# Kernel optimization log

Hardware: AMD Instinct MI355X
Metric: run time of the kernel (lower is better)

The kernel has to match this reference:

```python
import jax, jax.numpy as jnp
import numpy as np

B, N, D = 64, 512, 768


def setup_inputs() -> dict:
    key = jax.random.key(0)
    k = jax.random.split(key, 7)
    x = jax.random.normal(k[0], (B, N, D), dtype=jnp.float32)
    adj = jax.random.normal(k[1], (B, N, N), dtype=jnp.float32)
    # additive BERT-style mask: 0 for valid tokens, -10000 for padding
    lengths = jax.random.randint(k[2], (B,), N // 2, N + 1)
    valid = jnp.arange(N)[None, :] < lengths[:, None]          # [B, N]
    mask = jnp.where(valid, 0.0, -10000.0).astype(jnp.float32).reshape(B, 1, 1, N)
    roots_label = (jax.random.uniform(k[3], (B, N)) < 0.1).astype(jnp.float32)
    root_mask = valid.astype(jnp.int32)
    w_root = jax.random.normal(k[4], (D,), dtype=jnp.float32) / np.sqrt(D)
    b_root = jnp.zeros((), dtype=jnp.float32)
    return {"x": x, "adj": adj, "mask": mask, "roots_label": roots_label,
            "root_mask": root_mask, "w_root": w_root, "b_root": b_root}


def _matrix_tree_multi(scores, root):
    # scores: [B,N,N], root: [B,N]
    A = jnp.exp(scores)
    R = jnp.exp(root)
    L = jnp.sum(A, axis=1)                     # column sums (torch dim=1)
    LL = jnp.zeros_like(A).at[:, jnp.arange(A.shape[1]), jnp.arange(A.shape[1])].set(L + R) - A
    # equivalent to diag(L) - A + diag(R); keep diag of -A zeroed by set:
    LL = (jnp.apply_along_axis(jnp.diag, 1, np.zeros((1,))) if False else LL)  # no-op
    LL = jax.vmap(jnp.diag)(L + R) - A + jax.vmap(jnp.diag)(jnp.diagonal(A, axis1=1, axis2=2))
    # Recompute cleanly to match torch exactly: LL = diag(L) - A + diag(R)
    LL = jax.vmap(jnp.diag)(L) - A + jax.vmap(jnp.diag)(R)
    LL_inv = jnp.linalg.inv(LL)                # [B,N,N]
    LL_inv_diag = jnp.diagonal(LL_inv, axis1=1, axis2=2)   # [B,N]
    d0 = R * LL_inv_diag                       # root marginals [B,N]
    tmp1 = A * LL_inv_diag[:, None, :]         # A[i,j] * diag[j]
    tmp2 = A * jnp.swapaxes(LL_inv, 1, 2)      # A[i,j] * LL_inv[j,i]
    d = tmp1 - tmp2                            # edge marginals [B,N,N]
    return d, d0


def reference(x, adj, mask, roots_label, root_mask, w_root, b_root):
    root = jnp.einsum("bnd,d->bn", x, w_root) + b_root          # [B,N]
    m = mask[:, 0] / -10000.0                                    # [B,1,N], 0 valid / 1 pad
    root = jnp.maximum(root - m[:, 0, :] * 50.0, -40.0)
    scores = adj - m * 50.0 - jnp.swapaxes(m, 1, 2) * 50.0
    scores = jnp.maximum(scores, -40.0)
    d, d0 = _matrix_tree_multi(scores, root)
    # BCE root loss
    active = root_mask.reshape(-1) == 1
    labels = jnp.where(active, roots_label.reshape(-1), 0.0).astype(jnp.float32)
    logits = jnp.clip(d0.reshape(-1), 1e-5, 1.0 - 1e-5).astype(jnp.float32)
    bce = -(labels * jnp.log(logits) + (1.0 - labels) * jnp.log(1.0 - logits))
    loss_root = jnp.mean(bce * root_mask.reshape(-1).astype(jnp.float32))
    # attention = d^T with padded key columns zeroed
    attn = jnp.swapaxes(d, 1, 2)
    pad = jnp.broadcast_to(m.astype(bool), scores.shape)         # [B,N,N]
    attn = jnp.where(pad, 0.0, attn)
    context = jnp.matmul(attn, x)                                # [B,N,D]
    return context, d, loss_root
```

## Files before the change

### kernel.cpp

```cpp
#include <hip/hip_runtime.h>
#include <cstdint>
#include <cstddef>

#define BB 64
#define NN 512
#define DD 768
#define KB 64
#define NSTEP (NN/KB)

typedef __bf16 bf16x8 __attribute__((ext_vector_type(8)));
typedef float f32x4 __attribute__((ext_vector_type(4)));
typedef unsigned short us8 __attribute__((ext_vector_type(8)));
typedef double f64x4 __attribute__((ext_vector_type(4)));
typedef double f64x2 __attribute__((ext_vector_type(2)));

__device__ __forceinline__ float aval(float adjv, float mi, float mj) {
    return expf(fmaxf(adjv - 50.f * (mi + mj), -40.f));
}

__device__ __forceinline__ unsigned short f2bf(float v) {
    union { float f; unsigned int u; } c; c.f = v;
    return (unsigned short)((c.u + 0x7fffu + ((c.u >> 16) & 1u)) >> 16);
}
__device__ __forceinline__ float bf2f(unsigned short h) {
    union { unsigned int u; float f; } c; c.u = ((unsigned int)h) << 16;
    return c.f;
}

__device__ __forceinline__ void gl_lds16(const void* g, void* l) {
    __builtin_amdgcn_global_load_lds((const __attribute__((address_space(1))) unsigned int*)g,
                                     (__attribute__((address_space(3))) unsigned int*)l, 16, 0, 0);
}

__global__ void k_root(const float* __restrict__ x, const float* __restrict__ mask,
                       const float* __restrict__ w, const float* __restrict__ br,
                       float* __restrict__ R) {
    int wave = threadIdx.x >> 6, lane = threadIdx.x & 63;
    int row = blockIdx.x * 4 + wave;
    const float* xr = x + (size_t)row * DD;
    float s = 0.f;
#pragma unroll
    for (int k = 0; k < DD / 64; ++k) s += xr[k * 64 + lane] * w[k * 64 + lane];
    for (int off = 32; off; off >>= 1) s += __shfl_down(s, off, 64);
    if (lane == 0) {
        float m = mask[row] * -1e-4f;
        float rv = fmaxf(s + br[0] - 50.f * m, -40.f);
        R[row] = expf(rv);
    }
}

__global__ void k_colsum(const float* __restrict__ adj, const float* __restrict__ mask,
                         double* __restrict__ Lp) {
    int b = blockIdx.x, chunk = blockIdx.y;
    int j = threadIdx.x;
    float mj = mask[b * NN + j] * -1e-4f;
    const float* ab = adj + (size_t)b * NN * NN;
    double acc = 0.0;
    int i0 = chunk * 128;
    for (int i = i0; i < i0 + 128; ++i) {
        float mi = mask[b * NN + i] * -1e-4f;
        acc += (double)aval(ab[(size_t)i * NN + j], mi, mj);
    }
    Lp[((size_t)b * 4 + chunk) * NN + j] = acc;
}

template <typename T>
__global__ void k_build(const float* __restrict__ adj, const float* __restrict__ mask,
                        const float* __restrict__ R, const double* __restrict__ Lp,
                        T* __restrict__ M) {
    int b = blockIdx.x >> 9;
    int r = blockIdx.x & 511;
    int c = threadIdx.x;
    float mr = mask[b * NN + r] * -1e-4f;
    float mc = mask[b * NN + c] * -1e-4f;
    size_t idx = ((size_t)b * NN + r) * NN + c;
    float a = aval(adj[idx], mr, mc);
    T v;
    if (r == c) {
        const double* lp = Lp + (size_t)b * 4 * NN;
        double L = lp[c] + lp[NN + c] + lp[2 * NN + c] + lp[3 * NN + c];
        v = (T)(L - (double)a + (double)R[b * NN + c]);
    } else {
        v = (T)(-a);
    }
    M[idx] = v;
}

template <typename T>
__global__ void k_savecol(const T* __restrict__ M, T* __restrict__ Cb, int k0) {
    int t = threadIdx.x;
    int c = t & 63, rr = t >> 6;
    int row = blockIdx.x * 4 + rr;
    int b = row >> 9, i = row & 511;
    Cb[(size_t)row * KB + c] = M[((size_t)b * NN + i) * NN + k0 + c];
}

template <typename T>
__global__ void k_invblk(const T* __restrict__ M, T* __restrict__ Bb, int k0) {
    __shared__ double pr[KB];
    __shared__ double fv[KB];
    __shared__ double pvt;
    int b = blockIdx.x;
    int r = threadIdx.x & 63, q = threadIdx.x >> 6;
    double a[16];
    const T* Mb = M + ((size_t)b * NN + k0) * NN + k0;
#pragma unroll
    for (int c = 0; c < 16; ++c) a[c] = (double)Mb[(size_t)r * NN + q * 16 + c];
    for (int k = 0; k < KB; ++k) {
        int kq = k >> 4, kc = k & 15;
        if (r == k && q == kq) pvt = a[kc];
        __syncthreads();
        double ip = 1.0 / pvt;
        if (r == k) {
#pragma unroll
            for (int c = 0; c < 16; ++c) a[c] *= ip;
            if (q == kq) a[kc] = ip;
#pragma unroll
            for (int c = 0; c < 16; ++c) pr[q * 16 + c] = a[c];
        }
        if (r != k && q == kq) fv[r] = a[kc];
        __syncthreads();
        if (r != k) {
            double f = fv[r];
#pragma unroll
            for (int c = 0; c < 16; ++c) a[c] -= f * pr[q * 16 + c];
            if (q == kq) a[kc] = -f * ip;
        }
        __syncthreads();
    }
    T* Bo = Bb + (size_t)b * KB * KB;
#pragma unroll
    for (int c = 0; c < 16; ++c) Bo[r * KB + q * 16 + c] = (T)a[c];
}

__global__ __launch_bounds__(256) void k_piv_mfma(double* __restrict__ M,
                                                  const double* __restrict__ Bb, int step) {
    __shared__ double Ms[64][66];
    int b = blockIdx.y, jt = blockIdx.x;
    int t = threadIdx.x, w = t >> 6, l = t & 63;
    double* Mb = M + (size_t)b * NN * NN;
    double* Pr = Mb + (size_t)(step * 64) * NN;
    const double* Bi = Bb + (size_t)b * KB * KB;
    if (jt == step) {
        for (int i = 0; i < 16; ++i) {
            int c = i * 256 + t;
            int row = c >> 6, col = c & 63;
            Pr[(size_t)row * NN + step * 64 + col] = Bi[row * 64 + col];
        }
        return;
    }
    const double* Mg = Pr + jt * 64;
    for (int i = 0; i < 8; ++i) {
        int c = i * 256 + t;
        int row = c >> 5, ch = c & 31;
        f64x2 v = *(const f64x2*)(Mg + (size_t)row * NN + ch * 2);
        Ms[row][ch * 2] = v[0]; Ms[row][ch * 2 + 1] = v[1];
    }
    __syncthreads();
    int lr = l & 15, lg = l >> 4;
    double a[16];
#pragma unroll
    for (int kk = 0; kk < 16; ++kk) a[kk] = Bi[(w * 16 + lr) * 64 + kk * 4 + lg];
    double* Og = Pr + (size_t)(w * 16) * NN + jt * 64;
#pragma unroll
    for (int cf = 0; cf < 4; ++cf) {
        f64x4 acc = {0., 0., 0., 0.};
#pragma unroll
        for (int kk = 0; kk < 16; ++kk)
            acc = __builtin_amdgcn_mfma_f64_16x16x4f64(a[kk], Ms[kk * 4 + lg][cf * 16 + lr], acc, 0, 0, 0);
#pragma unroll
        for (int r = 0; r < 4; ++r) Og[(size_t)(lg + 4 * r) * NN + cf * 16 + lr] = acc[r];
    }
}

__global__ __launch_bounds__(256) void k_upd2(double* __restrict__ M,
                                              const double* __restrict__ Bb, int step) {
    __shared__ double Ts[64][66];
    int b = blockIdx.y;
    int x = blockIdx.x;
    int it = x >> 1, half = x & 1;
    if (it >= step) ++it;
    int t = threadIdx.x, w = t >> 6, l = t & 63;
    double* Mb = M + (size_t)b * NN * NN;
    {
        const double* Cg = Mb + (size_t)(it * 64) * NN + step * 64;
        for (int i = 0; i < 8; ++i) {
            int c = i * 256 + t;
            int row = c >> 5, ch = c & 31;
            f64x2 v = *(const f64x2*)(Cg + (size_t)row * NN + ch * 2);
            Ts[row][ch * 2] = -v[0]; Ts[row][ch * 2 + 1] = -v[1];
        }
    }
    __syncthreads();
    int lr = l & 15, lg = l >> 4;
    double a[16];
#pragma unroll
    for (int kk = 0; kk < 16; ++kk) a[kk] = Ts[w * 16 + lr][kk * 4 + lg];
    __syncthreads();
    int nj = half ? 3 : 4;
    for (int jj = 0; jj < nj; ++jj) {
        int jtidx = half ? 4 + jj : jj;
        int jt = (jtidx < step) ? jtidx : jtidx + 1;
        const double* Rg = Mb + (size_t)(step * 64) * NN + jt * 64;
        for (int i = 0; i < 8; ++i) {
            int c = i * 256 + t;
            int row = c >> 5, ch = c & 31;
            f64x2 v = *(const f64x2*)(Rg + (size_t)row * NN + ch * 2);
            Ts[row][ch * 2] = v[0]; Ts[row][ch * 2 + 1] = v[1];
        }
        __syncthreads();
        double* Og = Mb + (size_t)(it * 64 + w * 16) * NN + jt * 64;
#pragma unroll
        for (int cf = 0; cf < 4; ++cf) {
            int c0 = cf * 16 + lr;
            f64x4 acc;
#pragma unroll
            for (int r = 0; r < 4; ++r) acc[r] = Og[(size_t)(lg + 4 * r) * NN + c0];
#pragma unroll
            for (int kk = 0; kk < 16; ++kk)
                acc = __builtin_amdgcn_mfma_f64_16x16x4f64(a[kk], Ts[kk * 4 + lg][c0], acc, 0, 0, 0);
#pragma unroll
            for (int r = 0; r < 4; ++r) Og[(size_t)(lg + 4 * r) * NN + c0] = acc[r];
        }
        __syncthreads();
    }
    if (half) {
        const double* Bi = Bb + (size_t)b * KB * KB;
        for (int i = 0; i < 8; ++i) {
            int c = i * 256 + t;
            int row = c >> 5, ch = c & 31;
            f64x2 v = *(const f64x2*)(Bi + row * 64 + ch * 2);
            Ts[row][ch * 2] = v[0]; Ts[row][ch * 2 + 1] = v[1];
        }
        __syncthreads();
        double* Og = Mb + (size_t)(it * 64 + w * 16) * NN + step * 64;
#pragma unroll
        for (int cf = 0; cf < 4; ++cf) {
            int c0 = cf * 16 + lr;
            f64x4 acc = {0., 0., 0., 0.};
#pragma unroll
            for (int kk = 0; kk < 16; ++kk)
                acc = __builtin_amdgcn_mfma_f64_16x16x4f64(a[kk], Ts[kk * 4 + lg][c0], acc, 0, 0, 0);
#pragma unroll
            for (int r = 0; r < 4; ++r) Og[(size_t)(lg + 4 * r) * NN + c0] = acc[r];
        }
    }
}

template <typename T>
__global__ void k_pivrows(T* __restrict__ M, const T* __restrict__ Bb, int k0) {
    __shared__ double Bi[KB][KB];
    __shared__ double Mt[KB][KB + 1];
    int b = blockIdx.x, jt = blockIdx.y * 64;
    const T* Bo = Bb + (size_t)b * KB * KB;
    T* Mb = M + ((size_t)b * NN + k0) * NN;
    int t = threadIdx.x;
    for (int e = t; e < KB * KB; e += 256) {
        int rr = e >> 6, cc = e & 63;
        Bi[rr][cc] = (double)Bo[e];
        Mt[rr][cc] = (double)Mb[(size_t)rr * NN + jt + cc];
    }
    __syncthreads();
    if (blockIdx.y == (unsigned)(k0 >> 6)) {
        for (int e = t; e < KB * KB; e += 256) {
            int rr = e >> 6, cc = e & 63;
            Mb[(size_t)rr * NN + jt + cc] = (T)Bi[rr][cc];
        }
        return;
    }
    int tx = t & 15, ty = t >> 4;
    double acc[4][4] = {};
    for (int k = 0; k < KB; ++k) {
        double av[4], bv[4];
#pragma unroll
        for (int u = 0; u < 4; ++u) { av[u] = Bi[ty * 4 + u][k]; bv[u] = Mt[k][tx * 4 + u]; }
#pragma unroll
        for (int u = 0; u < 4; ++u)
#pragma unroll
            for (int v = 0; v < 4; ++v) acc[u][v] += av[u] * bv[v];
    }
#pragma unroll
    for (int u = 0; u < 4; ++u)
#pragma unroll
        for (int v = 0; v < 4; ++v)
            Mb[(size_t)(ty * 4 + u) * NN + jt + tx * 4 + v] = (T)acc[u][v];
}

template <typename T>
__global__ void k_update(T* __restrict__ M, const T* __restrict__ Cb, int k0) {
    int step = k0 >> 6;
    int it = blockIdx.y;
    if (it == step) return;
    int b = blockIdx.x, jt = blockIdx.z;
    __shared__ double Ct[KB][KB + 1];
    __shared__ double Rt[KB][KB + 1];
    int t = threadIdx.x;
    const T* Cbb = Cb + ((size_t)b * NN + it * 64) * KB;
    const T* Rb  = M + ((size_t)b * NN + k0) * NN + jt * 64;
    for (int e = t; e < KB * KB; e += 256) {
        int rr = e >> 6, cc = e & 63;
        Ct[rr][cc] = (double)Cbb[(size_t)rr * KB + cc];
        Rt[rr][cc] = (double)Rb[(size_t)rr * NN + cc];
    }
    __syncthreads();
    int tx = t & 15, ty = t >> 4;
    double acc[4][4] = {};
    for (int k = 0; k < KB; ++k) {
        double av[4], bv[4];
#pragma unroll
        for (int u = 0; u < 4; ++u) { av[u] = Ct[ty * 4 + u][k]; bv[u] = Rt[k][tx * 4 + u]; }
#pragma unroll
        for (int u = 0; u < 4; ++u)
#pragma unroll
            for (int v = 0; v < 4; ++v) acc[u][v] += av[u] * bv[v];
    }
    T* Mo = M + ((size_t)b * NN + it * 64) * NN + jt * 64;
    bool blockcol = (jt == step);
#pragma unroll
    for (int u = 0; u < 4; ++u) {
        int row = ty * 4 + u;
#pragma unroll
        for (int v = 0; v < 4; ++v) {
            int col = tx * 4 + v;
            double val = (double)Mo[(size_t)row * NN + col] - acc[u][v];
            if (blockcol) val -= Ct[row][col];
            Mo[(size_t)row * NN + col] = (T)val;
        }
    }
}

template <typename T>
__global__ void k_dgloss(const T* __restrict__ M, const float* __restrict__ R,
                         const float* __restrict__ rlab, const int* __restrict__ rmask,
                         double* __restrict__ Dg, float* __restrict__ lossp) {
    int idx = blockIdx.x * 256 + threadIdx.x;
    int b = idx >> 9, n = idx & 511;
    double xv = (double)M[((size_t)b * NN + n) * NN + n];
    Dg[idx] = xv;
    float d0 = R[idx] * (float)xv;
    float lg = fminf(fmaxf(d0, 1e-5f), 1.f - 1e-5f);
    float rm = (float)rmask[idx];
    float lab = (rmask[idx] == 1) ? rlab[idx] : 0.f;
    float bce = -(lab * logf(lg) + (1.f - lab) * logf(1.f - lg));
    __shared__ double sm[256];
    sm[threadIdx.x] = (double)(bce * rm);
    __syncthreads();
    for (int s = 128; s; s >>= 1) {
        if (threadIdx.x < s) sm[threadIdx.x] += sm[threadIdx.x + s];
        __syncthreads();
    }
    if (threadIdx.x == 0) lossp[blockIdx.x] = (float)sm[0];
}

__global__ void k_lossfin(const float* __restrict__ lossp, float* __restrict__ outv) {
    __shared__ double sm[128];
    sm[threadIdx.x] = (double)lossp[threadIdx.x];
    __syncthreads();
    for (int s = 64; s; s >>= 1) {
        if (threadIdx.x < s) sm[threadIdx.x] += sm[threadIdx.x + s];
        __syncthreads();
    }
    if (threadIdx.x == 0) outv[0] = (float)(sm[0] / (double)(BB * NN));
}

template <typename T>
__global__ void k_d(const T* __restrict__ M, const double* __restrict__ Dg,
                    const float* __restrict__ adj, const float* __restrict__ mask,
                    float* __restrict__ dout) {
    int b = blockIdx.x, i0 = blockIdx.y * 64, j0 = blockIdx.z * 64;
    __shared__ double Xt[64][65];
    int t = threadIdx.x, ii = t & 63, jj0 = t >> 6;
    const T* Mb = M + (size_t)b * NN * NN;
    for (int jj = jj0; jj < 64; jj += 4)
        Xt[jj][ii] = (double)Mb[(size_t)(j0 + jj) * NN + i0 + ii];
    __syncthreads();
    int jc = t & 63, ir0 = t >> 6;
    float mj = mask[b * NN + j0 + jc] * -1e-4f;
    double dg = Dg[b * NN + j0 + jc];
    const float* ab = adj + (size_t)b * NN * NN;
    float* db = dout + (size_t)b * NN * NN;
    for (int ir = ir0; ir < 64; ir += 4) {
        int i = i0 + ir;
        float mi = mask[b * NN + i] * -1e-4f;
        float a = aval(ab[(size_t)i * NN + j0 + jc], mi, mj);
        db[(size_t)i * NN + j0 + jc] = a * (float)(dg - Xt[jc][ir]);
    }
}

template <typename T>
__global__ void k_d2(const T* __restrict__ M, const double* __restrict__ Dg,
                     const float* __restrict__ adj, const float* __restrict__ mask,
                     float* __restrict__ dout,
                     unsigned short* __restrict__ ATh, unsigned short* __restrict__ ATl) {
    int b = blockIdx.x, i0 = blockIdx.y * 64, j0 = blockIdx.z * 64;
    __shared__ float Xt[64][65];
    __shared__ float dt[64][65];
    int t = threadIdx.x, ii = t & 63, jj0 = t >> 6;
    const T* Mb = M + (size_t)b * NN * NN;
    for (int jj = jj0; jj < 64; jj += 4)
        Xt[jj][ii] = (float)Mb[(size_t)(j0 + jj) * NN + i0 + ii];
    __syncthreads();
    int jc = t & 63, ir0 = t >> 6;
    float mj = mask[b * NN + j0 + jc] * -1e-4f;
    double dg = Dg[b * NN + j0 + jc];
    const float* ab = adj + (size_t)b * NN * NN;
    float* db = dout + (size_t)b * NN * NN;
    for (int ir = ir0; ir < 64; ir += 4) {
        int i = i0 + ir;
        float mi = mask[b * NN + i] * -1e-4f;
        float a = aval(ab[(size_t)i * NN + j0 + jc], mi, mj);
        float v = a * (float)(dg - (double)Xt[jc][ir]);
        db[(size_t)i * NN + j0 + jc] = v;
        dt[ir][jc] = v;
    }
    __syncthreads();
    int ql = t >> 2, kq = t & 3;
    us8 vh0, vh1, vl0, vl1;
#pragma unroll
    for (int u = 0; u < 16; ++u) {
        int k = kq * 16 + u;
        float mk = mask[b * NN + i0 + k] * -1e-4f;
        float v = (mk > 0.5f) ? 0.f : dt[k][ql];
        unsigned short h = f2bf(v);
        unsigned short lo = f2bf(v - bf2f(h));
        if (u < 8) { vh0[u] = h; vl0[u] = lo; } else { vh1[u - 8] = h; vl1[u - 8] = lo; }
    }
    size_t ao = ((size_t)b * NN + j0 + ql) * NN + i0 + kq * 16;
    *(us8*)&ATh[ao] = vh0; *(us8*)&ATh[ao + 8] = vh1;
    *(us8*)&ATl[ao] = vl0; *(us8*)&ATl[ao + 8] = vl1;
}

__global__ void k_cvt_x(const float* __restrict__ x,
                        unsigned short* __restrict__ XTh, unsigned short* __restrict__ XTl) {
    int b = blockIdx.x, k0 = blockIdx.y * 64, c0 = blockIdx.z * 64;
    __shared__ float xs[64][65];
    int t = threadIdx.x;
#pragma unroll
    for (int rep = 0; rep < 16; ++rep) {
        int e = rep * 256 + t;
        int row = e >> 6, col = e & 63;
        xs[row][col] = x[((size_t)b * NN + k0 + row) * DD + c0 + col];
    }
    __syncthreads();
    int cl = t >> 2, kq = t & 3;
    us8 vh0, vh1, vl0, vl1;
#pragma unroll
    for (int u = 0; u < 16; ++u) {
        int k = kq * 16 + u;
        float v = xs[k][cl];
        unsigned short h = f2bf(v);
        unsigned short lo = f2bf(v - bf2f(h));
        if (u < 8) { vh0[u] = h; vl0[u] = lo; } else { vh1[u - 8] = h; vl1[u - 8] = lo; }
    }
    size_t ao = ((size_t)b * DD + c0 + cl) * NN + k0 + kq * 16;
    *(us8*)&XTh[ao] = vh0; *(us8*)&XTh[ao + 8] = vh1;
    *(us8*)&XTl[ao] = vl0; *(us8*)&XTl[ao + 8] = vl1;
}

__global__ __launch_bounds__(256) void k_ctx3(const unsigned short* __restrict__ ATh,
                                              const unsigned short* __restrict__ ATl,
                                              const unsigned short* __restrict__ XTh,
                                              const unsigned short* __restrict__ XTl,
                                              float* __restrict__ ctx) {
    __shared__ __align__(16) unsigned short ABs[128 * 64];
    __shared__ __align__(16) unsigned short Xs[128 * 64];
    int b = blockIdx.x;
    int bm = blockIdx.y * 128, bn = blockIdx.z * 128;
    int t = threadIdx.x, wid = t >> 6, lane = t & 63;
    f32x4 acc[4][4];
#pragma unroll
    for (int i = 0; i < 4; ++i)
#pragma unroll
        for (int j = 0; j < 4; ++j) acc[i][j] = (f32x4){0.f, 0.f, 0.f, 0.f};

    const unsigned short* Agh = ATh + ((size_t)b * NN + bm) * NN;
    const unsigned short* Agl = ATl + ((size_t)b * NN + bm) * NN;
    const unsigned short* Xgh = XTh + ((size_t)b * DD + bn) * NN;
    const unsigned short* Xgl = XTl + ((size_t)b * DD + bn) * NN;

    int m0 = (wid >> 1) * 64, n0 = (wid & 1) * 64;
    int kc = lane >> 4;

    for (int kt = 0; kt < 16; ++kt) {
        int ki = kt * 32;
        __syncthreads();
#pragma unroll
        for (int it2 = 0; it2 < 4; ++it2) {
            int chunk = it2 * 256 + wid * 64 + lane;
            int row = chunk >> 3;
            int gs = (chunk & 7) ^ (row & 7);
            const unsigned short* s = (gs < 4) ? Agh + (size_t)row * NN + ki + gs * 8
                                               : Agl + (size_t)row * NN + ki + (gs - 4) * 8;
            gl_lds16(s, &ABs[(it2 * 256 + wid * 64) * 8]);
        }
#pragma unroll
        for (int it2 = 0; it2 < 4; ++it2) {
            int chunk = it2 * 256 + wid * 64 + lane;
            int row = chunk >> 3;
            int gs = (chunk & 7) ^ (row & 7);
            const unsigned short* s = (gs < 4) ? Xgh + (size_t)row * NN + ki + gs * 8
                                               : Xgl + (size_t)row * NN + ki + (gs - 4) * 8;
            gl_lds16(s, &Xs[(it2 * 256 + wid * 64) * 8]);
        }
        __syncthreads();
        bf16x8 ah[4], al[4], xh[4], xl[4];
#pragma unroll
        for (int f = 0; f < 4; ++f) {
            int ar = m0 + f * 16 + (lane & 15);
            ah[f] = *(const bf16x8*)&ABs[(ar * 8 + (kc ^ (ar & 7))) * 8];
            al[f] = *(const bf16x8*)&ABs[(ar * 8 + ((kc | 4) ^ (ar & 7))) * 8];
            int br = n0 + f * 16 + (lane & 15);
            xh[f] = *(const bf16x8*)&Xs[(br * 8 + (kc ^ (br & 7))) * 8];
            xl[f] = *(const bf16x8*)&Xs[(br * 8 + ((kc | 4) ^ (br & 7))) * 8];
        }
#pragma unroll
        for (int fm = 0; fm < 4; ++fm)
#pragma unroll
            for (int fn = 0; fn < 4; ++fn) {
                acc[fm][fn] = __builtin_amdgcn_mfma_f32_16x16x32_bf16(ah[fm], xh[fn], acc[fm][fn], 0, 0, 0);
                acc[fm][fn] = __builtin_amdgcn_mfma_f32_16x16x32_bf16(ah[fm], xl[fn], acc[fm][fn], 0, 0, 0);
                acc[fm][fn] = __builtin_amdgcn_mfma_f32_16x16x32_bf16(al[fm], xh[fn], acc[fm][fn], 0, 0, 0);
            }
    }
    float* cb = ctx + ((size_t)b * NN + bm + m0) * DD + bn + n0;
#pragma unroll
    for (int fm = 0; fm < 4; ++fm)
#pragma unroll
        for (int fn = 0; fn < 4; ++fn)
#pragma unroll
            for (int r = 0; r < 4; ++r) {
                int row = fm * 16 + (lane >> 4) * 4 + r;
                int col = fn * 16 + (lane & 15);
                cb[(size_t)row * DD + col] = acc[fm][fn][r];
            }
}

__global__ void k_ctx(const float* __restrict__ dmat, const float* __restrict__ x,
                      const float* __restrict__ mask, float* __restrict__ ctx) {
    int b = blockIdx.x, i0 = blockIdx.y * 64, c0 = blockIdx.z * 64;
    __shared__ float At[32][65];
    __shared__ float Xl[32][65];
    int t = threadIdx.x;
    int tx = t & 15, ty = t >> 4;
    float acc[4][4] = {};
    const float* db = dmat + (size_t)b * NN * NN;
    const float* xb = x + (size_t)b * NN * DD;
    int li = t & 63, lk = t >> 6;
    for (int kt = 0; kt < NN; kt += 32) {
#pragma unroll
        for (int rep = 0; rep < 8; ++rep) {
            int kk = lk + rep * 4;
            float mk = mask[b * NN + kt + kk] * -1e-4f;
            float v = db[(size_t)(kt + kk) * NN + i0 + li];
            At[kk][li] = (mk > 0.5f) ? 0.f : v;
            Xl[kk][li] = xb[(size_t)(kt + kk) * DD + c0 + li];
        }
        __syncthreads();
        for (int kk = 0; kk < 32; ++kk) {
            float av[4], bv[4];
#pragma unroll
            for (int u = 0; u < 4; ++u) { av[u] = At[kk][ty * 4 + u]; bv[u] = Xl[kk][tx * 4 + u]; }
#pragma unroll
            for (int u = 0; u < 4; ++u)
#pragma unroll
                for (int v = 0; v < 4; ++v) acc[u][v] += av[u] * bv[v];
        }
        __syncthreads();
    }
    float* cb = ctx + (size_t)b * NN * DD;
#pragma unroll
    for (int u = 0; u < 4; ++u)
#pragma unroll
        for (int v = 0; v < 4; ++v)
            cb[(size_t)(i0 + ty * 4 + u) * DD + c0 + tx * 4 + v] = acc[u][v];
}

template <typename T>
static void run_old(const float* x, const float* adj, const float* mask,
                    const float* rlab, const int* rmask, const float* w, const float* br,
                    float* ctx, float* dmat, float* lossout,
                    char* ws, hipStream_t stream) {
    size_t off = 0;
    T* M  = (T*)(ws + off); off += (size_t)BB * NN * NN * sizeof(T);
    T* Cb = (T*)(ws + off); off += (size_t)BB * NN * KB * sizeof(T);
    T* Bb = (T*)(ws + off); off += (size_t)BB * KB * KB * sizeof(T);
    double* Lp = (double*)(ws + off); off += (size_t)BB * 4 * NN * 8;
    float* Rf  = (float*)(ws + off);  off += (size_t)BB * NN * 4;
    double* Dg = (double*)(ws + off); off += (size_t)BB * NN * 8;
    float* lossp = (float*)(ws + off);

    k_root<<<BB * NN / 4, 256, 0, stream>>>(x, mask, w, br, Rf);
    k_colsum<<<dim3(BB, 4), 512, 0, stream>>>(adj, mask, Lp);
    k_build<T><<<BB * NN, 512, 0, stream>>>(adj, mask, Rf, Lp, M);
    for (int s = 0; s < NSTEP; ++s) {
        int k0 = s * KB;
        k_savecol<T><<<BB * NN / 4, 256, 0, stream>>>(M, Cb, k0);
        k_invblk<T><<<BB, 256, 0, stream>>>(M, Bb, k0);
        k_pivrows<T><<<dim3(BB, 8), 256, 0, stream>>>(M, Bb, k0);
        k_update<T><<<dim3(BB, 8, 8), 256, 0, stream>>>(M, Cb, k0);
    }
    k_dgloss<T><<<BB * NN / 256, 256, 0, stream>>>(M, Rf, rlab, rmask, Dg, lossp);
    k_lossfin<<<1, 128, 0, stream>>>(lossp, lossout);
    k_d<T><<<dim3(BB, 8, 8), 256, 0, stream>>>(M, Dg, adj, mask, dmat);
    k_ctx<<<dim3(BB, 8, 12), 256, 0, stream>>>(dmat, x, mask, ctx);
}

static void run_new(const float* x, const float* adj, const float* mask,
                    const float* rlab, const int* rmask, const float* w, const float* br,
                    float* ctx, float* dmat, float* lossout,
                    char* ws, hipStream_t stream) {
    size_t off = 0;
    double* M  = (double*)(ws + off); off += (size_t)BB * NN * NN * 8;
    double* Cb = (double*)(ws + off); off += (size_t)BB * NN * KB * 8;
    double* Bb = (double*)(ws + off); off += (size_t)BB * KB * KB * 8;
    double* Lp = (double*)(ws + off); off += (size_t)BB * 4 * NN * 8;
    float* Rf  = (float*)(ws + off);  off += (size_t)BB * NN * 4;
    double* Dg = (double*)(ws + off); off += (size_t)BB * NN * 8;
    float* lossp = (float*)(ws + off); off += 4096;
    unsigned short* ATh = (unsigned short*)(ws + off); off += (size_t)BB * NN * NN * 2;
    unsigned short* ATl = (unsigned short*)(ws + off); off += (size_t)BB * NN * NN * 2;
    unsigned short* XTh = (unsigned short*)(ws);
    unsigned short* XTl = (unsigned short*)(ws + (size_t)BB * DD * NN * 2);
    (void)Cb;

    k_root<<<BB * NN / 4, 256, 0, stream>>>(x, mask, w, br, Rf);
    k_colsum<<<dim3(BB, 4), 512, 0, stream>>>(adj, mask, Lp);
    k_build<double><<<BB * NN, 512, 0, stream>>>(adj, mask, Rf, Lp, M);
    for (int s = 0; s < NSTEP; ++s) {
        k_invblk<double><<<BB, 256, 0, stream>>>(M, Bb, s * KB);
        k_piv_mfma<<<dim3(8, BB), 256, 0, stream>>>(M, Bb, s);
        k_upd2<<<dim3(14, BB), 256, 0, stream>>>(M, Bb, s);
    }
    k_dgloss<double><<<BB * NN / 256, 256, 0, stream>>>(M, Rf, rlab, rmask, Dg, lossp);
    k_lossfin<<<1, 128, 0, stream>>>(lossp, lossout);
    k_d2<double><<<dim3(BB, 8, 8), 256, 0, stream>>>(M, Dg, adj, mask, dmat, ATh, ATl);
    k_cvt_x<<<dim3(BB, 8, 12), 256, 0, stream>>>(x, XTh, XTl);
    k_ctx3<<<dim3(BB, 4, 6), 256, 0, stream>>>(ATh, ATl, XTh, XTl, ctx);
}

extern "C" void kernel_launch(void* const* d_in, const int* in_sizes, int n_in,
                              void* d_out, int out_size, void* d_ws, size_t ws_size,
                              hipStream_t stream) {
    const float* x    = (const float*)d_in[0];
    const float* adj  = (const float*)d_in[1];
    const float* mask = (const float*)d_in[2];
    const float* rlab = (const float*)d_in[3];
    const int*   rmask= (const int*)d_in[4];
    const float* w    = (const float*)d_in[5];
    const float* br   = (const float*)d_in[6];
    float* out = (float*)d_out;
    float* ctx = out;
    float* dmat = out + (size_t)BB * NN * DD;
    float* lossout = dmat + (size_t)BB * NN * NN;
    char* ws = (char*)d_ws;

    size_t base = (size_t)BB * NN * NN * 8 + (size_t)BB * NN * KB * 8 + (size_t)BB * KB * KB * 8
                + (size_t)BB * 4 * NN * 8 + (size_t)BB * NN * 4 + (size_t)BB * NN * 8 + 4096;
    size_t need_new = base + (size_t)BB * NN * NN * 4;
    if (ws_size >= need_new)
        run_new(x, adj, mask, rlab, rmask, w, br, ctx, dmat, lossout, ws, stream);
    else if (ws_size >= base)
        run_old<double>(x, adj, mask, rlab, rmask, w, br, ctx, dmat, lossout, ws, stream);
    else
        run_old<float>(x, adj, mask, rlab, rmask, w, br, ctx, dmat, lossout, ws, stream);
}
```

Before: 1.235 ms.

## Fuse diagonal block inversion into pivot kernel; double-buffer context GEMM loads

The per-step diagonal 64x64 block inversion kernel is removed. Every pivot-row block now redundantly inverts the diagonal block in registers and LDS before doing its MFMA multiply, and the jt==step block writes the inverse back. This drops one launch per step (8 launches) and the global round-trip of the inverse, at the cost of redundant Gauss-Jordan work across 8 blocks per batch. Separately, the context GEMM gets double-buffered LDS staging with explicit vmcnt waits so global loads overlap the MFMAs, and its grid is reordered so the batch index is the slowest dimension.

New measurement: 1.384 ms. 1.12x slower.

```diff
diff --git a/kernel.cpp b/kernel.cpp
--- a/kernel.cpp
+++ b/kernel.cpp
@@ -133,43 +133,80 @@
     for (int c = 0; c < 16; ++c) Bo[r * KB + q * 16 + c] = (T)a[c];
 }
 
-__global__ __launch_bounds__(256) void k_piv_mfma(double* __restrict__ M,
-                                                  const double* __restrict__ Bb, int step) {
+__global__ __launch_bounds__(256) void k_piv2(double* __restrict__ M,
+                                              double* __restrict__ Bb, int step) {
     __shared__ double Ms[64][66];
+    __shared__ double Bs[64][66];
+    __shared__ double pr[KB];
+    __shared__ double fv[KB];
+    __shared__ double pvt;
     int b = blockIdx.y, jt = blockIdx.x;
     int t = threadIdx.x, w = t >> 6, l = t & 63;
     double* Mb = M + (size_t)b * NN * NN;
     double* Pr = Mb + (size_t)(step * 64) * NN;
-    const double* Bi = Bb + (size_t)b * KB * KB;
-    if (jt == step) {
-        for (int i = 0; i < 16; ++i) {
+    if (jt != step) {
+        const double* Mg = Pr + jt * 64;
+        for (int i = 0; i < 8; ++i) {
             int c = i * 256 + t;
-            int row = c >> 6, col = c & 63;
-            Pr[(size_t)row * NN + step * 64 + col] = Bi[row * 64 + col];
-        }
-        return;
-    }
-    const double* Mg = Pr + jt * 64;
-    for (int i = 0; i < 8; ++i) {
-        int c = i * 256 + t;
-        int row = c >> 5, ch = c & 31;
-        f64x2 v = *(const f64x2*)(Mg + (size_t)row * NN + ch * 2);
-        Ms[row][ch * 2] = v[0]; Ms[row][ch * 2 + 1] = v[1];
+            int row = c >> 5, ch = c & 31;
+            f64x2 v = *(const f64x2*)(Mg + (size_t)row * NN + ch * 2);
+            Ms[row][ch * 2] = v[0]; Ms[row][ch * 2 + 1] = v[1];
+        }
+    }
+    {
+        int r = t & 63, q = t >> 6;
+        double a[16];
+        const double* Pp = Pr + step * 64;
+#pragma unroll
+        for (int c = 0; c < 16; ++c) a[c] = Pp[(size_t)r * NN + q * 16 + c];
+        for (int k = 0; k < KB; ++k) {
+            int kq = k >> 4, kc = k & 15;
+            if (r == k && q == kq) pvt = a[kc];
+            __syncthreads();
+            double ip = 1.0 / pvt;
+            if (r == k) {
+#pragma unroll
+                for (int c = 0; c < 16; ++c) a[c] *= ip;
+                if (q == kq) a[kc] = ip;
+#pragma unroll
+                for (int c = 0; c < 16; ++c) pr[q * 16 + c] = a[c];
+            }
+            if (r != k && q == kq) fv[r] = a[kc];
+            __syncthreads();
+            if (r != k) {
+                double f = fv[r];
+#pragma unroll
+                for (int c = 0; c < 16; ++c) a[c] -= f * pr[q * 16 + c];
+                if (q == kq) a[kc] = -f * ip;
+            }
+            __syncthreads();
+        }
+#pragma unroll
+        for (int c = 0; c < 16; ++c) Bs[r][q * 16 + c] = a[c];
+        if (jt == step) {
+            double* Bo = Bb + (size_t)b * KB * KB;
+#pragma unroll
+            for (int c = 0; c < 16; ++c) {
+                Bo[r * KB + q * 16 + c] = a[c];
+                Pr[(size_t)r * NN + step * 64 + q * 16 + c] = a[c];
+            }
+            return;
+        }
     }
     __syncthreads();
     int lr = l & 15, lg = l >> 4;
-    double a[16];
-#pragma unroll
-    for (int kk = 0; kk < 16; ++kk) a[kk] = Bi[(w * 16 + lr) * 64 + kk * 4 + lg];
+    double af[16];
+#pragma unroll
+    for (int kk = 0; kk < 16; ++kk) af[kk] = Bs[w * 16 + lr][kk * 4 + lg];
     double* Og = Pr + (size_t)(w * 16) * NN + jt * 64;
 #pragma unroll
     for (int cf = 0; cf < 4; ++cf) {
         f64x4 acc = {0., 0., 0., 0.};
 #pragma unroll
         for (int kk = 0; kk < 16; ++kk)
-            acc = __builtin_amdgcn_mfma_f64_16x16x4f64(a[kk], Ms[kk * 4 + lg][cf * 16 + lr], acc, 0, 0, 0);
-#pragma unroll
-        for (int r = 0; r < 4; ++r) Og[(size_t)(lg + 4 * r) * NN + cf * 16 + lr] = acc[r];
+            acc = __builtin_amdgcn_mfma_f64_16x16x4f64(af[kk], Ms[kk * 4 + lg][cf * 16 + lr], acc, 0, 0, 0);
+#pragma unroll
+        for (int r2 = 0; r2 < 4; ++r2) Og[(size_t)(lg + 4 * r2) * NN + cf * 16 + lr] = acc[r2];
     }
 }
 
@@ -457,15 +494,15 @@
     *(us8*)&XTl[ao] = vl0; *(us8*)&XTl[ao + 8] = vl1;
 }
 
-__global__ __launch_bounds__(256) void k_ctx3(const unsigned short* __restrict__ ATh,
+__global__ __launch_bounds__(256) void k_ctx4(const unsigned short* __restrict__ ATh,
                                               const unsigned short* __restrict__ ATl,
                                               const unsigned short* __restrict__ XTh,
                                               const unsigned short* __restrict__ XTl,
                                               float* __restrict__ ctx) {
-    __shared__ __align__(16) unsigned short ABs[128 * 64];
-    __shared__ __align__(16) unsigned short Xs[128 * 64];
-    int b = blockIdx.x;
-    int bm = blockIdx.y * 128, bn = blockIdx.z * 128;
+    __shared__ __align__(16) unsigned short ABs[2][128 * 64];
+    __shared__ __align__(16) unsigned short Xs[2][128 * 64];
+    int b = blockIdx.z;
+    int bm = blockIdx.y * 128, bn = blockIdx.x * 128;
     int t = threadIdx.x, wid = t >> 6, lane = t & 63;
     f32x4 acc[4][4];
 #pragma unroll
@@ -481,9 +518,8 @@
     int m0 = (wid >> 1) * 64, n0 = (wid & 1) * 64;
     int kc = lane >> 4;
 
-    for (int kt = 0; kt < 16; ++kt) {
+    auto STAGE = [&](int kt, int buf) {
         int ki = kt * 32;
-        __syncthreads();
 #pragma unroll
         for (int it2 = 0; it2 < 4; ++it2) {
             int chunk = it2 * 256 + wid * 64 + lane;
@@ -491,7 +527,7 @@
             int gs = (chunk & 7) ^ (row & 7);
             const unsigned short* s = (gs < 4) ? Agh + (size_t)row * NN + ki + gs * 8
                                                : Agl + (size_t)row * NN + ki + (gs - 4) * 8;
-            gl_lds16(s, &ABs[(it2 * 256 + wid * 64) * 8]);
+            gl_lds16(s, &ABs[buf][(it2 * 256 + wid * 64) * 8]);
         }
 #pragma unroll
         for (int it2 = 0; it2 < 4; ++it2) {
@@ -500,18 +536,29 @@
             int gs = (chunk & 7) ^ (row & 7);
             const unsigned short* s = (gs < 4) ? Xgh + (size_t)row * NN + ki + gs * 8
                                                : Xgl + (size_t)row * NN + ki + (gs - 4) * 8;
-            gl_lds16(s, &Xs[(it2 * 256 + wid * 64) * 8]);
-        }
-        __syncthreads();
+            gl_lds16(s, &Xs[buf][(it2 * 256 + wid * 64) * 8]);
+        }
+    };
+
+    STAGE(0, 0);
+    int cur = 0;
+    for (int kt = 0; kt < 16; ++kt) {
+        if (kt + 1 < 16) {
+            STAGE(kt + 1, cur ^ 1);
+            asm volatile("s_waitcnt vmcnt(8)" ::: "memory");
+        } else {
+            asm volatile("s_waitcnt vmcnt(0)" ::: "memory");
+        }
+        __builtin_amdgcn_s_barrier();
         bf16x8 ah[4], al[4], xh[4], xl[4];
 #pragma unroll
         for (int f = 0; f < 4; ++f) {
             int ar = m0 + f * 16 + (lane & 15);
-            ah[f] = *(const bf16x8*)&ABs[(ar * 8 + (kc ^ (ar & 7))) * 8];
-            al[f] = *(const bf16x8*)&ABs[(ar * 8 + ((kc | 4) ^ (ar & 7))) * 8];
+            ah[f] = *(const bf16x8*)&ABs[cur][(ar * 8 + (kc ^ (ar & 7))) * 8];
+            al[f] = *(const bf16x8*)&ABs[cur][(ar * 8 + ((kc | 4) ^ (ar & 7))) * 8];
             int br = n0 + f * 16 + (lane & 15);
-            xh[f] = *(const bf16x8*)&Xs[(br * 8 + (kc ^ (br & 7))) * 8];
-            xl[f] = *(const bf16x8*)&Xs[(br * 8 + ((kc | 4) ^ (br & 7))) * 8];
+            xh[f] = *(const bf16x8*)&Xs[cur][(br * 8 + (kc ^ (br & 7))) * 8];
+            xl[f] = *(const bf16x8*)&Xs[cur][(br * 8 + ((kc | 4) ^ (br & 7))) * 8];
         }
 #pragma unroll
         for (int fm = 0; fm < 4; ++fm)
@@ -521,6 +568,8 @@
                 acc[fm][fn] = __builtin_amdgcn_mfma_f32_16x16x32_bf16(ah[fm], xl[fn], acc[fm][fn], 0, 0, 0);
                 acc[fm][fn] = __builtin_amdgcn_mfma_f32_16x16x32_bf16(al[fm], xh[fn], acc[fm][fn], 0, 0, 0);
             }
+        __builtin_amdgcn_s_barrier();
+        cur ^= 1;
     }
     float* cb = ctx + ((size_t)b * NN + bm + m0) * DD + bn + n0;
 #pragma unroll
@@ -627,15 +676,14 @@
     k_colsum<<<dim3(BB, 4), 512, 0, stream>>>(adj, mask, Lp);
     k_build<double><<<BB * NN, 512, 0, stream>>>(adj, mask, Rf, Lp, M);
     for (int s = 0; s < NSTEP; ++s) {
-        k_invblk<double><<<BB, 256, 0, stream>>>(M, Bb, s * KB);
-        k_piv_mfma<<<dim3(8, BB), 256, 0, stream>>>(M, Bb, s);
+        k_piv2<<<dim3(8, BB), 256, 0, stream>>>(M, Bb, s);
         k_upd2<<<dim3(14, BB), 256, 0, stream>>>(M, Bb, s);
     }
     k_dgloss<double><<<BB * NN / 256, 256, 0, stream>>>(M, Rf, rlab, rmask, Dg, lossp);
     k_lossfin<<<1, 128, 0, stream>>>(lossp, lossout);
     k_d2<double><<<dim3(BB, 8, 8), 256, 0, stream>>>(M, Dg, adj, mask, dmat, ATh, ATl);
     k_cvt_x<<<dim3(BB, 8, 12), 256, 0, stream>>>(x, XTh, XTl);
-    k_ctx3<<<dim3(BB, 4, 6), 256, 0, stream>>>(ATh, ATl, XTh, XTl, ctx);
+    k_ctx4<<<dim3(6, 4, BB), 256, 0, stream>>>(ATh, ATl, XTh, XTl, ctx);
 }
 
 extern "C" void kernel_launch(void* const* d_in, const int* in_sizes, int n_in,
```

## Double-buffer ctx GEMM LDS loads and remap block IDs across XCDs

Applied to the files above, without the earlier changes.

The context GEMM now double-buffers its LDS tiles, issuing the next k-tile's global-to-LDS loads before computing on the current one, with explicit vmcnt waits and barriers in place of the two syncthreads per iteration. The pivot-row, trailing-update and ctx kernels switch to 1D grids with a block-index swizzle. The swizzle is meant to keep blocks of the same batch on the same XCD and share its L2. Doubling LDS use may lower occupancy, and the hand-written vmcnt count depends on how many loads the compiler issues per stage.

Result: faster. 1.177 ms (-4.7%).

```diff
diff --git a/kernel.cpp b/kernel.cpp
--- a/kernel.cpp
+++ b/kernel.cpp
@@ -136,7 +136,9 @@
 __global__ __launch_bounds__(256) void k_piv_mfma(double* __restrict__ M,
                                                   const double* __restrict__ Bb, int step) {
     __shared__ double Ms[64][66];
-    int b = blockIdx.y, jt = blockIdx.x;
+    int o = blockIdx.x;
+    int g = (o & 7) * 64 + (o >> 3);
+    int b = g >> 3, jt = g & 7;
     int t = threadIdx.x, w = t >> 6, l = t & 63;
     double* Mb = M + (size_t)b * NN * NN;
     double* Pr = Mb + (size_t)(step * 64) * NN;
@@ -176,8 +178,10 @@
 __global__ __launch_bounds__(256) void k_upd2(double* __restrict__ M,
                                               const double* __restrict__ Bb, int step) {
     __shared__ double Ts[64][66];
-    int b = blockIdx.y;
-    int x = blockIdx.x;
+    int o = blockIdx.x;
+    int g = (o & 7) * 112 + (o >> 3);
+    int b = g / 14;
+    int x = g % 14;
     int it = x >> 1, half = x & 1;
     if (it >= step) ++it;
     int t = threadIdx.x, w = t >> 6, l = t & 63;
@@ -457,15 +461,18 @@
     *(us8*)&XTl[ao] = vl0; *(us8*)&XTl[ao + 8] = vl1;
 }
 
-__global__ __launch_bounds__(256) void k_ctx3(const unsigned short* __restrict__ ATh,
+__global__ __launch_bounds__(256) void k_ctx5(const unsigned short* __restrict__ ATh,
                                               const unsigned short* __restrict__ ATl,
                                               const unsigned short* __restrict__ XTh,
                                               const unsigned short* __restrict__ XTl,
                                               float* __restrict__ ctx) {
-    __shared__ __align__(16) unsigned short ABs[128 * 64];
-    __shared__ __align__(16) unsigned short Xs[128 * 64];
-    int b = blockIdx.x;
-    int bm = blockIdx.y * 128, bn = blockIdx.z * 128;
+    __shared__ __align__(16) unsigned short ABs[2][128 * 64];
+    __shared__ __align__(16) unsigned short Xs[2][128 * 64];
+    int o = blockIdx.x;
+    int g = (o & 7) * 192 + (o >> 3);
+    int b = g / 24;
+    int rem = g % 24;
+    int bm = (rem / 6) * 128, bn = (rem % 6) * 128;
     int t = threadIdx.x, wid = t >> 6, lane = t & 63;
     f32x4 acc[4][4];
 #pragma unroll
@@ -481,9 +488,8 @@
     int m0 = (wid >> 1) * 64, n0 = (wid & 1) * 64;
     int kc = lane >> 4;
 
-    for (int kt = 0; kt < 16; ++kt) {
+    auto STAGE = [&](int kt, int buf) {
         int ki = kt * 32;
-        __syncthreads();
 #pragma unroll
         for (int it2 = 0; it2 < 4; ++it2) {
             int chunk = it2 * 256 + wid * 64 + lane;
@@ -491,7 +497,7 @@
             int gs = (chunk & 7) ^ (row & 7);
             const unsigned short* s = (gs < 4) ? Agh + (size_t)row * NN + ki + gs * 8
                                                : Agl + (size_t)row * NN + ki + (gs - 4) * 8;
-            gl_lds16(s, &ABs[(it2 * 256 + wid * 64) * 8]);
+            gl_lds16(s, &ABs[buf][(it2 * 256 + wid * 64) * 8]);
         }
 #pragma unroll
         for (int it2 = 0; it2 < 4; ++it2) {
@@ -500,18 +506,29 @@
             int gs = (chunk & 7) ^ (row & 7);
             const unsigned short* s = (gs < 4) ? Xgh + (size_t)row * NN + ki + gs * 8
                                                : Xgl + (size_t)row * NN + ki + (gs - 4) * 8;
-            gl_lds16(s, &Xs[(it2 * 256 + wid * 64) * 8]);
-        }
-        __syncthreads();
+            gl_lds16(s, &Xs[buf][(it2 * 256 + wid * 64) * 8]);
+        }
+    };
+
+    STAGE(0, 0);
+    int cur = 0;
+    for (int kt = 0; kt < 16; ++kt) {
+        if (kt + 1 < 16) {
+            STAGE(kt + 1, cur ^ 1);
+            asm volatile("s_waitcnt vmcnt(8)" ::: "memory");
+        } else {
+            asm volatile("s_waitcnt vmcnt(0)" ::: "memory");
+        }
+        __builtin_amdgcn_s_barrier();
         bf16x8 ah[4], al[4], xh[4], xl[4];
 #pragma unroll
         for (int f = 0; f < 4; ++f) {
             int ar = m0 + f * 16 + (lane & 15);
-            ah[f] = *(const bf16x8*)&ABs[(ar * 8 + (kc ^ (ar & 7))) * 8];
-            al[f] = *(const bf16x8*)&ABs[(ar * 8 + ((kc | 4) ^ (ar & 7))) * 8];
+            ah[f] = *(const bf16x8*)&ABs[cur][(ar * 8 + (kc ^ (ar & 7))) * 8];
+            al[f] = *(const bf16x8*)&ABs[cur][(ar * 8 + ((kc | 4) ^ (ar & 7))) * 8];
             int br = n0 + f * 16 + (lane & 15);
-            xh[f] = *(const bf16x8*)&Xs[(br * 8 + (kc ^ (br & 7))) * 8];
-            xl[f] = *(const bf16x8*)&Xs[(br * 8 + ((kc | 4) ^ (br & 7))) * 8];
+            xh[f] = *(const bf16x8*)&Xs[cur][(br * 8 + (kc ^ (br & 7))) * 8];
+            xl[f] = *(const bf16x8*)&Xs[cur][(br * 8 + ((kc | 4) ^ (br & 7))) * 8];
         }
 #pragma unroll
         for (int fm = 0; fm < 4; ++fm)
@@ -521,6 +538,8 @@
                 acc[fm][fn] = __builtin_amdgcn_mfma_f32_16x16x32_bf16(ah[fm], xl[fn], acc[fm][fn], 0, 0, 0);
                 acc[fm][fn] = __builtin_amdgcn_mfma_f32_16x16x32_bf16(al[fm], xh[fn], acc[fm][fn], 0, 0, 0);
             }
+        __builtin_amdgcn_s_barrier();
+        cur ^= 1;
     }
     float* cb = ctx + ((size_t)b * NN + bm + m0) * DD + bn + n0;
 #pragma unroll
@@ -628,14 +647,14 @@
     k_build<double><<<BB * NN, 512, 0, stream>>>(adj, mask, Rf, Lp, M);
     for (int s = 0; s < NSTEP; ++s) {
         k_invblk<double><<<BB, 256, 0, stream>>>(M, Bb, s * KB);
-        k_piv_mfma<<<dim3(8, BB), 256, 0, stream>>>(M, Bb, s);
-        k_upd2<<<dim3(14, BB), 256, 0, stream>>>(M, Bb, s);
+        k_piv_mfma<<<512, 256, 0, stream>>>(M, Bb, s);
+        k_upd2<<<896, 256, 0, stream>>>(M, Bb, s);
     }
     k_dgloss<double><<<BB * NN / 256, 256, 0, stream>>>(M, Rf, rlab, rmask, Dg, lossp);
     k_lossfin<<<1, 128, 0, stream>>>(lossp, lossout);
     k_d2<double><<<dim3(BB, 8, 8), 256, 0, stream>>>(M, Dg, adj, mask, dmat, ATh, ATl);
     k_cvt_x<<<dim3(BB, 8, 12), 256, 0, stream>>>(x, XTh, XTl);
-    k_ctx3<<<dim3(BB, 4, 6), 256, 0, stream>>>(ATh, ATl, XTh, XTl, ctx);
+    k_ctx5<<<1536, 256, 0, stream>>>(ATh, ATl, XTh, XTl, ctx);
 }
 
 extern "C" void kernel_launch(void* const* d_in, const int* in_sizes, int n_in,
```
